# Kernel tuning notes

Hardware: AMD Instinct MI355X
Metric: run time of the kernel (lower is better)

The kernel has to match this reference:

```python
import jax, jax.numpy as jnp
import numpy as np
import math

SQRT2 = math.sqrt(2.0)


def _rotation_grids(theta_deg, grid_size):
    # torch affine_grid (align_corners=True) base coords for output [G, G]:
    # grid[h, w] = (xs[w], ys[h]) transformed by R = [[c, s, 0], [-s, c, 0]]
    xs = jnp.linspace(-1.0, 1.0, grid_size, dtype=jnp.float32)
    X, Y = jnp.meshgrid(xs, xs)            # [G,G], X varies along width
    th = jnp.deg2rad(theta_deg.astype(jnp.float32))[:, None, None]  # [T,1,1]
    c, s = jnp.cos(th), jnp.sin(th)
    gx = c * X + s * Y                      # [T,G,G]
    gy = -s * X + c * Y
    return gx, gy


def _bilinear_sample(x, gx, gy):
    # x: [N,C,H,W]; gx,gy: [T,G,G] normalized coords in [-1,1]
    # bilinear, zeros padding, align_corners=True -> returns [N,C,T,G,G]
    N, C, H, W = x.shape
    ix = (gx + 1.0) * 0.5 * (W - 1)
    iy = (gy + 1.0) * 0.5 * (H - 1)
    ix0 = jnp.floor(ix)
    iy0 = jnp.floor(iy)
    wx1 = ix - ix0
    wy1 = iy - iy0
    wx0 = 1.0 - wx1
    wy0 = 1.0 - wy1

    def gather(iyf, ixf):
        valid = (ixf >= 0) & (ixf <= W - 1) & (iyf >= 0) & (iyf <= H - 1)
        ii = jnp.clip(ixf, 0, W - 1).astype(jnp.int32)
        jj = jnp.clip(iyf, 0, H - 1).astype(jnp.int32)
        v = x[:, :, jj, ii]                 # [N,C,T,G,G]
        return v * valid.astype(x.dtype)

    return (gather(iy0, ix0) * (wy0 * wx0)
            + gather(iy0, ix0 + 1) * (wy0 * wx1)
            + gather(iy0 + 1, ix0) * (wy1 * wx0)
            + gather(iy0 + 1, ix0 + 1) * (wy1 * wx1))


def radon_forward(x, theta_deg):
    N, C, W, H = x.shape
    # circle=False: pad image to the diagonal size so rotations keep all content
    diagonal = SQRT2 * W
    pad = int(math.ceil(diagonal - W))
    new_center = (W + pad) // 2
    old_center = W // 2
    pad_before = new_center - old_center
    x = jnp.pad(x, ((0, 0), (0, 0), (pad_before, pad - pad_before),
                    (pad_before, pad - pad_before)))
    G = x.shape[-1]                         # padded grid size == ceil(sqrt2*W)
    gx, gy = _rotation_grids(theta_deg, G)  # [T,G,G]
    rotated = _bilinear_sample(x, gx, gy)   # [N,C,T,G,G]
    sino = rotated.sum(axis=3)              # integrate over rows -> [N,C,T,G]
    return jnp.swapaxes(sino, 2, 3)         # [N,C,G,T]


def setup_inputs() -> dict:
    key = jax.random.key(0)
    x = jax.random.normal(key, (2, 1, 256, 256), dtype=jnp.float32)
    theta = jnp.arange(180, dtype=jnp.int64) if jax.config.jax_enable_x64 else jnp.arange(180, dtype=jnp.int32)
    return {"x": x, "theta": theta}


def reference(x, theta):
    return radon_forward(x, theta)
```

## Files before the change

### kernel.cpp

```cpp
#include <hip/hip_runtime.h>
#include <hip/hip_fp16.h>
#include <math.h>


#define G       363
#define NT      180
#define PADB    53
#define STEP    (2.0f / 362.0f)
#define DEG2RAD 0.017453292519943295f

#define TS2     64
#define TROWS   68
#define NCHK    17
#define NTILE   (NCHK * 256)
#define NJB     12
#define NIB     8
#define NJBF    6
#define CW      264
#define CH      264
#define NTUPLE  (90 * NJB * NIB)

#define GLOAD16(gp, lp) __builtin_amdgcn_global_load_lds(                     \
    (const __attribute__((address_space(1))) void*)(gp),                      \
    (__attribute__((address_space(3))) void*)(lp), 16, 0, 0)

__global__ __launch_bounds__(256) void radon_fwd(
    const float* __restrict__ x, const int* __restrict__ theta,
    float* __restrict__ out)
{
    const int t = blockIdx.x / NJBF, jb = blockIdx.x % NJBF;
    const int jl = threadIdx.x, chunk = threadIdx.y;
    const int j = jb * 64 + jl;
    const float th = (float)theta[t] * DEG2RAD;
    const float c = cosf(th), s = sinf(th);
    const float xj = fmaf((float)j, STEP, -1.0f);
    const float s181 = s * 181.0f, c181 = c * 181.0f;
    const float bx = fmaf(c, xj, 1.0f) * 181.0f;
    const float by = fmaf(-s, xj, 1.0f) * 181.0f;
    const float* img0 = x;
    const float* img1 = x + 65536;
    float acc0 = 0.f, acc1 = 0.f;
    for (int i = chunk; i < G; i += 4) {
        const float xi = fmaf((float)i, STEP, -1.0f);
        const float ix = fmaf(s181, xi, bx);
        const float iy = fmaf(c181, xi, by);
        const float fx = floorf(ix), fy = floorf(iy);
        const int ix0 = (int)fx, iy0 = (int)fy;
        const float wx1 = ix - fx, wy1 = iy - fy;
        const float wx0 = 1.f - wx1, wy0 = 1.f - wy1;
        const int cc0 = ix0 - 53, cc1 = cc0 + 1, rr0 = iy0 - 53, rr1 = rr0 + 1;
        const float wxa = ((unsigned)cc0 < 256u) ? wx0 : 0.f;
        const float wxb = ((unsigned)cc1 < 256u) ? wx1 : 0.f;
        const float wya = ((unsigned)rr0 < 256u) ? wy0 : 0.f;
        const float wyb = ((unsigned)rr1 < 256u) ? wy1 : 0.f;
        const int c0c = min(max(cc0, 0), 255), c1c = min(max(cc1, 0), 255);
        const int r0b = min(max(rr0, 0), 255) << 8, r1b = min(max(rr1, 0), 255) << 8;
        const float w00 = wya * wxa, w01 = wya * wxb, w10 = wyb * wxa, w11 = wyb * wxb;
        acc0 = fmaf(img0[r0b + c0c], w00, acc0);
        acc0 = fmaf(img0[r0b + c1c], w01, acc0);
        acc0 = fmaf(img0[r1b + c0c], w10, acc0);
        acc0 = fmaf(img0[r1b + c1c], w11, acc0);
        acc1 = fmaf(img1[r0b + c0c], w00, acc1);
        acc1 = fmaf(img1[r0b + c1c], w01, acc1);
        acc1 = fmaf(img1[r1b + c0c], w10, acc1);
        acc1 = fmaf(img1[r1b + c1c], w11, acc1);
    }
    __shared__ float red[2][4][64];
    red[0][chunk][jl] = acc0;
    red[1][chunk][jl] = acc1;
    __syncthreads();
    if (threadIdx.y < 2 && j < G) {
        const int n = threadIdx.y;
        out[n * (G * NT) + j * NT + t] =
            red[n][0][jl] + red[n][1][jl] + red[n][2][jl] + red[n][3][jl];
    }
}

__global__ __launch_bounds__(256) void prep_k(
    const float* __restrict__ x, const int* __restrict__ theta,
    unsigned* __restrict__ xIh, unsigned* __restrict__ xTIh,
    int4* __restrict__ bbox, float* __restrict__ out)
{
    const int bid = blockIdx.x;
    const int tx = threadIdx.x, ty = threadIdx.y;
    const int tid = ty * 32 + tx;

    if (bid < 81) {
        __shared__ unsigned tl[32][33];
        const int cx0 = (bid % 9) * 32, cy0 = (bid / 9) * 32;
        #pragma unroll
        for (int dy = 0; dy < 32; dy += 8) {
            const int cy = cy0 + ty + dy, cx = cx0 + tx;
            const int pr = cy - 4, pc = cx - 4;
            unsigned v = 0u;
            if ((unsigned)pr < 256u && (unsigned)pc < 256u) {
                const int p = pr * 256 + pc;
                const unsigned short a = __half_as_ushort(__float2half_rn(x[p]));
                const unsigned short b = __half_as_ushort(__float2half_rn(x[p + 65536]));
                v = (unsigned)a | ((unsigned)b << 16);
            }
            if (cy < CH && cx < CW) xIh[cy * CW + cx] = v;
            tl[ty + dy][tx] = v;
        }
        __syncthreads();
        #pragma unroll
        for (int dy = 0; dy < 32; dy += 8) {
            const int rp = cx0 + ty + dy, cp = cy0 + tx;
            if (rp < CH && cp < CW) xTIh[rp * CW + cp] = tl[tx][ty + dy];
        }
    } else if (bid < 115) {
        const int tuple = (bid - 81) * 256 + tid;
        if (tuple < NTUPLE) {
            const int tg  = tuple / (NJB * NIB), rem = tuple - tg * (NJB * NIB);
            const int jb  = rem / NIB,   ib  = rem - jb * NIB;
            const float thA = (float)theta[tg * 2]     * DEG2RAD;
            const float thB = (float)theta[tg * 2 + 1] * DEG2RAD;
            const float cA = cosf(thA), sA = sinf(thA);
            const float cB = cosf(thB), sB = sinf(thB);
            const float xjm = fmaf((float)(jb * 32),      STEP, -1.0f);
            const float xjM = fmaf((float)(jb * 32 + 31), STEP, -1.0f);
            const float xim = fmaf((float)(ib * 48),      STEP, -1.0f);
            const float xiM = fmaf((float)(ib * 48 + 47), STEP, -1.0f);
            float ixmin = 1e30f, ixmax = -1e30f, iymin = 1e30f, iymax = -1e30f;
            #pragma unroll
            for (int qq = 0; qq < 8; ++qq) {
                const float cc  = (qq & 4) ? cB : cA;
                const float ss  = (qq & 4) ? sB : sA;
                const float xjc = (qq & 1) ? xjM : xjm;
                const float xic = (qq & 2) ? xiM : xim;
                const float bxq = fmaf(cc,  xjc, 1.0f) * 181.0f;
                const float byq = fmaf(-ss, xjc, 1.0f) * 181.0f;
                const float ixq = fmaf(ss * 181.0f, xic, bxq);
                const float iyq = fmaf(cc * 181.0f, xic, byq);
                ixmin = fminf(ixmin, ixq); ixmax = fmaxf(ixmax, ixq);
                iymin = fminf(iymin, iyq); iymax = fmaxf(iymax, iyq);
            }
            const int caseA = (fabsf(cA) + fabsf(cB) >= fabsf(sA) + fabsf(sB));
            const float Umin = caseA ? iymin : ixmin;
            const float Umax = caseA ? iymax : ixmax;
            const float Vmin = caseA ? ixmin : iymin;
            const int r0 = (int)floorf(Umin) - 1;
            const int c0 = (int)floorf(Vmin) - 1;
            int rows = (int)floorf(Umax) - (int)floorf(Umin) + 4;
            rows = min(rows, TROWS);
            const int nchunk = (rows + 3) >> 2;
            const int r0p = r0 - PADB, c0p = c0 - PADB;
            const int tyLast = (nchunk * 256 - 1) >> 6;
            const int safe = (r0p >= -4) && (r0p + tyLast <= 259)
                          && (c0p >= -4) && (c0p <= 196);
            bbox[tuple] = make_int4(r0p, c0p,
                                    nchunk | (safe << 8) | (caseA << 9),
                                    0);
        }
    } else {
        const int idx = (bid - 115) * 256 + tid;
        if (idx < 32670) ((float4*)out)[idx] = make_float4(0.f, 0.f, 0.f, 0.f);
    }
}

template<bool SAFE>
__device__ __forceinline__ void stage_direct(unsigned* tileB,
    const unsigned* __restrict__ srcC,
    int r0p, int c0p, int nchunk, int wid, int lane)
{
    const int B = (r0p + 4) * CW + (c0p + 4);
    for (int h = wid; h < nchunk; h += 4) {
        const int hs   = __builtin_amdgcn_readfirstlane(h);
        const int cell = (hs << 8) + (lane << 2);
        const int tyc  = cell >> 6;
        const int txc  = cell & 63;
        int idx;
        if (SAFE) {
            idx = tyc * CW + txc + B;
        } else {
            const int rc = min(max(r0p + tyc, -4), 256) + 4;
            const int cc = min(max(c0p + txc, -4), 256) + 4;
            idx = rc * CW + cc;
        }
        GLOAD16(srcC + idx, (char*)tileB + (hs << 10));
    }
}

template<bool TAIL>
__device__ __forceinline__ void gather6(const unsigned* __restrict__ tl,
    float Uf0, float Vf0, float dU, float dV, int iexc,
    float& a0, float& a1)
{
    __half2 acc = __float2half2_rn(0.0f);
    #pragma unroll
    for (int k = 0; k < 6; ++k) {
        const float Uf = fmaf((float)k, dU, Uf0);
        const float Vf = fmaf((float)k, dV, Vf0);
        const float fU = floorf(Uf), fV = floorf(Vf);
        const float wU1 = Uf - fU;
        const float wV1 = Vf - fV;
        const int rel = (int)fmaf(fU, (float)TS2, fV);
        const __half2 x00 = *(const __half2*)(tl + rel);
        const __half2 x01 = *(const __half2*)(tl + rel + 1);
        const __half2 x10 = *(const __half2*)(tl + rel + TS2);
        const __half2 x11 = *(const __half2*)(tl + rel + TS2 + 1);
        const __half2 wv2 = __float2half2_rn(wV1);
        const __half2 wu2 = __float2half2_rn(wU1);
        const __half2 t0 = __hfma2(wv2, __hsub2(x01, x00), x00);
        const __half2 t1 = __hfma2(wv2, __hsub2(x11, x10), x10);
        __half2 v = __hfma2(wu2, __hsub2(t1, t0), t0);
        if (TAIL && k >= iexc) v = __float2half2_rn(0.0f);
        acc = __hadd2(acc, v);
    }
    a0 += __low2float(acc);
    a1 += __high2float(acc);
}

__global__ __launch_bounds__(256) void radon_tile7(
    const unsigned* __restrict__ xIh, const unsigned* __restrict__ xTIh,
    const int*   __restrict__ theta, const int4* __restrict__ bbox,
    float* __restrict__ out)
{
    __shared__ unsigned tile[NTILE];

    const int blk  = blockIdx.x;
    const int z    = blockIdx.y;
    const int tg   = blk / NJB;
    const int jb   = blk - tg * NJB;
    const int tid  = threadIdx.x;
    const int lane = tid & 63;
    const int wid  = tid >> 6;
    const int a    = wid >> 1;
    const int wj   = wid & 1;
    const int jl   = lane & 15;
    const int kk   = lane >> 4;

    const int t = tg * 2 + a;
    const float th = (float)theta[t] * DEG2RAD;
    const float c = cosf(th), s = sinf(th);
    const float s181 = s * 181.0f, c181 = c * 181.0f;

    const int   j  = jb * 32 + wj * 16 + jl;
    const float xj = fmaf((float)j, STEP, -1.0f);
    const float bx = fmaf(c,  xj, 1.0f) * 181.0f;
    const float by = fmaf(-s, xj, 1.0f) * 181.0f;

    const float fiofs = (float)(kk * 12);

    const int tb = (tg * NJB + jb) * NIB + z * 4;
    const int caseA = (__builtin_amdgcn_readfirstlane(bbox[tb].z) >> 9) & 1;
    const unsigned* __restrict__ srcC = caseA ? xIh : xTIh;

    const float slopeU = caseA ? c181 : s181;
    const float slopeV = caseA ? s181 : c181;
    const float dU = slopeU * STEP;
    const float dV = slopeV * STEP;
    const float U00 = (caseA ? by : bx) - slopeU;
    const float V00 = (caseA ? bx : by) - slopeV;

    float a0 = 0.f, a1 = 0.f;

    #pragma unroll
    for (int ibi = 0; ibi < 4; ++ibi) {
        const int ib = z * 4 + ibi;
        const int4 bb = bbox[tb + ibi];
        const int r0p    = __builtin_amdgcn_readfirstlane(bb.x);
        const int c0p    = __builtin_amdgcn_readfirstlane(bb.y);
        const int flags  = __builtin_amdgcn_readfirstlane(bb.z);
        const int nchunk = flags & 255;
        const int safe   = (flags >> 8) & 1;

        __syncthreads();

        if (safe) stage_direct<true >(tile, srcC, r0p, c0p, nchunk, wid, lane);
        else      stage_direct<false>(tile, srcC, r0p, c0p, nchunk, wid, lane);
        __syncthreads();

        const int i0 = ib * 48;
        const float r0f = (float)(r0p + PADB);
        const float c0f = (float)(c0p + PADB);
        const float fi  = (float)i0 + fiofs;
        const float Uf1 = fmaf(dU, fi, U00) - r0f;
        const float Vf1 = fmaf(dV, fi, V00) - c0f;
        const float Uf2 = fmaf(dU, 6.0f, Uf1);
        const float Vf2 = fmaf(dV, 6.0f, Vf1);
        const int ibase = i0 + kk * 12;

        if (i0 + 47 < G) {
            gather6<false>(tile, Uf1, Vf1, dU, dV, 6, a0, a1);
            gather6<false>(tile, Uf2, Vf2, dU, dV, 6, a0, a1);
        } else {
            gather6<true>(tile, Uf1, Vf1, dU, dV, G - ibase,     a0, a1);
            gather6<true>(tile, Uf2, Vf2, dU, dV, G - ibase - 6, a0, a1);
        }
    }

    float vx = a0;
    float vy = a1;
    vx += __shfl_xor(vx, 16);
    vy += __shfl_xor(vy, 16);
    vx += __shfl_xor(vx, 32);
    vy += __shfl_xor(vy, 32);

    if (lane < 16 && j < G) {
        atomicAdd(&out[j * NT + t],          vx);
        atomicAdd(&out[G * NT + j * NT + t], vy);
    }
}

extern "C" void kernel_launch(void* const* d_in, const int* in_sizes, int n_in,
                              void* d_out, int out_size, void* d_ws, size_t ws_size,
                              hipStream_t stream) {
    const float* x     = (const float*)d_in[0];
    const int*   theta = (const int*)d_in[1];
    float*       out   = (float*)d_out;

    const size_t XIH_OFF  = 0;
    const size_t XTIH_OFF = (size_t)CH * CW * 4;
    const size_t BBOX_OFF = 2 * XTIH_OFF;
    const size_t NEED     = BBOX_OFF + (size_t)NTUPLE * 16;

    if (ws_size < NEED) {
        hipLaunchKernelGGL(radon_fwd, dim3(NT * NJBF), dim3(64, 4), 0, stream,
                           x, theta, out);
        return;
    }

    unsigned* xIh  = (unsigned*)((char*)d_ws + XIH_OFF);
    unsigned* xTIh = (unsigned*)((char*)d_ws + XTIH_OFF);
    int4*     bbox = (int4*)((char*)d_ws + BBOX_OFF);

    hipLaunchKernelGGL(prep_k, dim3(243), dim3(32, 8), 0, stream,
                       x, theta, xIh, xTIh, bbox, out);
    hipLaunchKernelGGL(radon_tile7, dim3(1080, 2), dim3(256), 0, stream,
                       xIh, xTIh, theta, bbox, out);
}
```

Baseline: 34.06 us.

## Replace LDS-tiled bbox staging with direct L2 gathers from padded half images

```diff
diff --git a/kernel.cpp b/kernel.cpp
--- a/kernel.cpp
+++ b/kernel.cpp
@@ -5,24 +5,13 @@
 
 #define G       363
 #define NT      180
-#define PADB    53
 #define STEP    (2.0f / 362.0f)
 #define DEG2RAD 0.017453292519943295f
 
-#define TS2     64
-#define TROWS   68
-#define NCHK    17
-#define NTILE   (NCHK * 256)
 #define NJB     12
-#define NIB     8
 #define NJBF    6
 #define CW      264
 #define CH      264
-#define NTUPLE  (90 * NJB * NIB)
-
-#define GLOAD16(gp, lp) __builtin_amdgcn_global_load_lds(                     \
-    (const __attribute__((address_space(1))) void*)(gp),                      \
-    (__attribute__((address_space(3))) void*)(lp), 16, 0, 0)
 
 __global__ __launch_bounds__(256) void radon_fwd(
     const float* __restrict__ x, const int* __restrict__ theta,
@@ -77,229 +66,133 @@
 }
 
 __global__ __launch_bounds__(256) void prep_k(
-    const float* __restrict__ x, const int* __restrict__ theta,
-    unsigned* __restrict__ xIh, unsigned* __restrict__ xTIh,
-    int4* __restrict__ bbox, float* __restrict__ out)
+    const float* __restrict__ x,
+    unsigned* __restrict__ xIh, unsigned* __restrict__ xTIh)
 {
     const int bid = blockIdx.x;
     const int tx = threadIdx.x, ty = threadIdx.y;
-    const int tid = ty * 32 + tx;
-
-    if (bid < 81) {
-        __shared__ unsigned tl[32][33];
-        const int cx0 = (bid % 9) * 32, cy0 = (bid / 9) * 32;
-        #pragma unroll
-        for (int dy = 0; dy < 32; dy += 8) {
-            const int cy = cy0 + ty + dy, cx = cx0 + tx;
-            const int pr = cy - 4, pc = cx - 4;
-            unsigned v = 0u;
-            if ((unsigned)pr < 256u && (unsigned)pc < 256u) {
-                const int p = pr * 256 + pc;
-                const unsigned short a = __half_as_ushort(__float2half_rn(x[p]));
-                const unsigned short b = __half_as_ushort(__float2half_rn(x[p + 65536]));
-                v = (unsigned)a | ((unsigned)b << 16);
-            }
-            if (cy < CH && cx < CW) xIh[cy * CW + cx] = v;
-            tl[ty + dy][tx] = v;
+
+    __shared__ unsigned tl[32][33];
+    const int cx0 = (bid % 9) * 32, cy0 = (bid / 9) * 32;
+    #pragma unroll
+    for (int dy = 0; dy < 32; dy += 8) {
+        const int cy = cy0 + ty + dy, cx = cx0 + tx;
+        const int pr = cy - 4, pc = cx - 4;
+        unsigned v = 0u;
+        if ((unsigned)pr < 256u && (unsigned)pc < 256u) {
+            const int p = pr * 256 + pc;
+            const unsigned short a = __half_as_ushort(__float2half_rn(x[p]));
+            const unsigned short b = __half_as_ushort(__float2half_rn(x[p + 65536]));
+            v = (unsigned)a | ((unsigned)b << 16);
         }
-        __syncthreads();
-        #pragma unroll
-        for (int dy = 0; dy < 32; dy += 8) {
-            const int rp = cx0 + ty + dy, cp = cy0 + tx;
-            if (rp < CH && cp < CW) xTIh[rp * CW + cp] = tl[tx][ty + dy];
-        }
-    } else if (bid < 115) {
-        const int tuple = (bid - 81) * 256 + tid;
-        if (tuple < NTUPLE) {
-            const int tg  = tuple / (NJB * NIB), rem = tuple - tg * (NJB * NIB);
-            const int jb  = rem / NIB,   ib  = rem - jb * NIB;
-            const float thA = (float)theta[tg * 2]     * DEG2RAD;
-            const float thB = (float)theta[tg * 2 + 1] * DEG2RAD;
-            const float cA = cosf(thA), sA = sinf(thA);
-            const float cB = cosf(thB), sB = sinf(thB);
-            const float xjm = fmaf((float)(jb * 32),      STEP, -1.0f);
-            const float xjM = fmaf((float)(jb * 32 + 31), STEP, -1.0f);
-            const float xim = fmaf((float)(ib * 48),      STEP, -1.0f);
-            const float xiM = fmaf((float)(ib * 48 + 47), STEP, -1.0f);
-            float ixmin = 1e30f, ixmax = -1e30f, iymin = 1e30f, iymax = -1e30f;
-            #pragma unroll
-            for (int qq = 0; qq < 8; ++qq) {
-                const float cc  = (qq & 4) ? cB : cA;
-                const float ss  = (qq & 4) ? sB : sA;
-                const float xjc = (qq & 1) ? xjM : xjm;
-                const float xic = (qq & 2) ? xiM : xim;
-                const float bxq = fmaf(cc,  xjc, 1.0f) * 181.0f;
-                const float byq = fmaf(-ss, xjc, 1.0f) * 181.0f;
-                const float ixq = fmaf(ss * 181.0f, xic, bxq);
-                const float iyq = fmaf(cc * 181.0f, xic, byq);
-                ixmin = fminf(ixmin, ixq); ixmax = fmaxf(ixmax, ixq);
-                iymin = fminf(iymin, iyq); iymax = fmaxf(iymax, iyq);
-            }
-            const int caseA = (fabsf(cA) + fabsf(cB) >= fabsf(sA) + fabsf(sB));
-            const float Umin = caseA ? iymin : ixmin;
-            const float Umax = caseA ? iymax : ixmax;
-            const float Vmin = caseA ? ixmin : iymin;
-            const int r0 = (int)floorf(Umin) - 1;
-            const int c0 = (int)floorf(Vmin) - 1;
-            int rows = (int)floorf(Umax) - (int)floorf(Umin) + 4;
-            rows = min(rows, TROWS);
-            const int nchunk = (rows + 3) >> 2;
-            const int r0p = r0 - PADB, c0p = c0 - PADB;
-            const int tyLast = (nchunk * 256 - 1) >> 6;
-            const int safe = (r0p >= -4) && (r0p + tyLast <= 259)
-                          && (c0p >= -4) && (c0p <= 196);
-            bbox[tuple] = make_int4(r0p, c0p,
-                                    nchunk | (safe << 8) | (caseA << 9),
-                                    0);
-        }
-    } else {
-        const int idx = (bid - 115) * 256 + tid;
-        if (idx < 32670) ((float4*)out)[idx] = make_float4(0.f, 0.f, 0.f, 0.f);
-    }
-}
-
-template<bool SAFE>
-__device__ __forceinline__ void stage_direct(unsigned* tileB,
-    const unsigned* __restrict__ srcC,
-    int r0p, int c0p, int nchunk, int wid, int lane)
-{
-    const int B = (r0p + 4) * CW + (c0p + 4);
-    for (int h = wid; h < nchunk; h += 4) {
-        const int hs   = __builtin_amdgcn_readfirstlane(h);
-        const int cell = (hs << 8) + (lane << 2);
-        const int tyc  = cell >> 6;
-        const int txc  = cell & 63;
-        int idx;
-        if (SAFE) {
-            idx = tyc * CW + txc + B;
-        } else {
-            const int rc = min(max(r0p + tyc, -4), 256) + 4;
-            const int cc = min(max(c0p + txc, -4), 256) + 4;
-            idx = rc * CW + cc;
-        }
-        GLOAD16(srcC + idx, (char*)tileB + (hs << 10));
-    }
-}
-
-template<bool TAIL>
-__device__ __forceinline__ void gather6(const unsigned* __restrict__ tl,
-    float Uf0, float Vf0, float dU, float dV, int iexc,
-    float& a0, float& a1)
-{
-    __half2 acc = __float2half2_rn(0.0f);
+        if (cy < CH && cx < CW) xIh[cy * CW + cx] = v;
+        tl[ty + dy][tx] = v;
+    }
+    __syncthreads();
     #pragma unroll
-    for (int k = 0; k < 6; ++k) {
-        const float Uf = fmaf((float)k, dU, Uf0);
-        const float Vf = fmaf((float)k, dV, Vf0);
-        const float fU = floorf(Uf), fV = floorf(Vf);
-        const float wU1 = Uf - fU;
-        const float wV1 = Vf - fV;
-        const int rel = (int)fmaf(fU, (float)TS2, fV);
-        const __half2 x00 = *(const __half2*)(tl + rel);
-        const __half2 x01 = *(const __half2*)(tl + rel + 1);
-        const __half2 x10 = *(const __half2*)(tl + rel + TS2);
-        const __half2 x11 = *(const __half2*)(tl + rel + TS2 + 1);
-        const __half2 wv2 = __float2half2_rn(wV1);
-        const __half2 wu2 = __float2half2_rn(wU1);
-        const __half2 t0 = __hfma2(wv2, __hsub2(x01, x00), x00);
-        const __half2 t1 = __hfma2(wv2, __hsub2(x11, x10), x10);
-        __half2 v = __hfma2(wu2, __hsub2(t1, t0), t0);
-        if (TAIL && k >= iexc) v = __float2half2_rn(0.0f);
-        acc = __hadd2(acc, v);
-    }
-    a0 += __low2float(acc);
-    a1 += __high2float(acc);
-}
-
-__global__ __launch_bounds__(256) void radon_tile7(
+    for (int dy = 0; dy < 32; dy += 8) {
+        const int rp = cx0 + ty + dy, cp = cy0 + tx;
+        if (rp < CH && cp < CW) xTIh[rp * CW + cp] = tl[tx][ty + dy];
+    }
+}
+
+__device__ __forceinline__ __half2 tap(const unsigned* __restrict__ cv,
+    float fi, float dU, float dV, float U00, float V00)
+{
+    const float U = fmaf(dU, fi, U00);
+    const float V = fmaf(dV, fi, V00);
+    const float fU = floorf(U), fV = floorf(V);
+    const float wU1 = U - fU, wV1 = V - fV;
+    const float fUc = fminf(fmaxf(fU, 0.0f), 262.0f);
+    const float fVc = fminf(fmaxf(fV, 0.0f), 262.0f);
+    const int rel = (int)fmaf(fUc, (float)CW, fVc);
+    const __half2* p = (const __half2*)(cv + rel);
+    const __half2 x00 = p[0];
+    const __half2 x01 = p[1];
+    const __half2 x10 = p[CW];
+    const __half2 x11 = p[CW + 1];
+    const __half2 wv2 = __float2half2_rn(wV1);
+    const __half2 wu2 = __float2half2_rn(wU1);
+    const __half2 t0 = __hfma2(wv2, __hsub2(x01, x00), x00);
+    const __half2 t1 = __hfma2(wv2, __hsub2(x11, x10), x10);
+    return __hfma2(wu2, __hsub2(t1, t0), t0);
+}
+
+__global__ __launch_bounds__(256) void radon_l2(
     const unsigned* __restrict__ xIh, const unsigned* __restrict__ xTIh,
-    const int*   __restrict__ theta, const int4* __restrict__ bbox,
-    float* __restrict__ out)
-{
-    __shared__ unsigned tile[NTILE];
-
+    const int* __restrict__ theta, float* __restrict__ out)
+{
     const int blk  = blockIdx.x;
-    const int z    = blockIdx.y;
-    const int tg   = blk / NJB;
-    const int jb   = blk - tg * NJB;
+    const int t    = blk / NJB;
+    const int jb   = blk - t * NJB;
     const int tid  = threadIdx.x;
     const int lane = tid & 63;
     const int wid  = tid >> 6;
-    const int a    = wid >> 1;
-    const int wj   = wid & 1;
-    const int jl   = lane & 15;
-    const int kk   = lane >> 4;
-
-    const int t = tg * 2 + a;
+    const int jl   = lane & 31;
+    const int kc   = lane >> 5;
+    const int chunk = wid * 2 + kc;
+
     const float th = (float)theta[t] * DEG2RAD;
     const float c = cosf(th), s = sinf(th);
     const float s181 = s * 181.0f, c181 = c * 181.0f;
 
-    const int   j  = jb * 32 + wj * 16 + jl;
+    const int   j  = jb * 32 + jl;
     const float xj = fmaf((float)j, STEP, -1.0f);
     const float bx = fmaf(c,  xj, 1.0f) * 181.0f;
     const float by = fmaf(-s, xj, 1.0f) * 181.0f;
 
-    const float fiofs = (float)(kk * 12);
-
-    const int tb = (tg * NJB + jb) * NIB + z * 4;
-    const int caseA = (__builtin_amdgcn_readfirstlane(bbox[tb].z) >> 9) & 1;
-    const unsigned* __restrict__ srcC = caseA ? xIh : xTIh;
+    const int caseA = (fabsf(c) >= fabsf(s));
+    const unsigned* __restrict__ cv = caseA ? xIh : xTIh;
 
     const float slopeU = caseA ? c181 : s181;
     const float slopeV = caseA ? s181 : c181;
     const float dU = slopeU * STEP;
     const float dV = slopeV * STEP;
-    const float U00 = (caseA ? by : bx) - slopeU;
-    const float V00 = (caseA ? bx : by) - slopeV;
+    const float U00 = (caseA ? by : bx) - slopeU - 49.0f;
+    const float V00 = (caseA ? bx : by) - slopeV - 49.0f;
 
     float a0 = 0.f, a1 = 0.f;
 
-    #pragma unroll
-    for (int ibi = 0; ibi < 4; ++ibi) {
-        const int ib = z * 4 + ibi;
-        const int4 bb = bbox[tb + ibi];
-        const int r0p    = __builtin_amdgcn_readfirstlane(bb.x);
-        const int c0p    = __builtin_amdgcn_readfirstlane(bb.y);
-        const int flags  = __builtin_amdgcn_readfirstlane(bb.z);
-        const int nchunk = flags & 255;
-        const int safe   = (flags >> 8) & 1;
-
-        __syncthreads();
-
-        if (safe) stage_direct<true >(tile, srcC, r0p, c0p, nchunk, wid, lane);
-        else      stage_direct<false>(tile, srcC, r0p, c0p, nchunk, wid, lane);
-        __syncthreads();
-
-        const int i0 = ib * 48;
-        const float r0f = (float)(r0p + PADB);
-        const float c0f = (float)(c0p + PADB);
-        const float fi  = (float)i0 + fiofs;
-        const float Uf1 = fmaf(dU, fi, U00) - r0f;
-        const float Vf1 = fmaf(dV, fi, V00) - c0f;
-        const float Uf2 = fmaf(dU, 6.0f, Uf1);
-        const float Vf2 = fmaf(dV, 6.0f, Vf1);
-        const int ibase = i0 + kk * 12;
-
-        if (i0 + 47 < G) {
-            gather6<false>(tile, Uf1, Vf1, dU, dV, 6, a0, a1);
-            gather6<false>(tile, Uf2, Vf2, dU, dV, 6, a0, a1);
-        } else {
-            gather6<true>(tile, Uf1, Vf1, dU, dV, G - ibase,     a0, a1);
-            gather6<true>(tile, Uf2, Vf2, dU, dV, G - ibase - 6, a0, a1);
+    float fig = (float)chunk;
+    for (int g = 0; g < 7; ++g) {
+        __half2 acc = __float2half2_rn(0.0f);
+        #pragma unroll
+        for (int k = 0; k < 6; ++k) {
+            acc = __hadd2(acc, tap(cv, fig + (float)(k * 8), dU, dV, U00, V00));
         }
-    }
-
-    float vx = a0;
-    float vy = a1;
-    vx += __shfl_xor(vx, 16);
-    vy += __shfl_xor(vy, 16);
-    vx += __shfl_xor(vx, 32);
-    vy += __shfl_xor(vy, 32);
-
-    if (lane < 16 && j < G) {
-        atomicAdd(&out[j * NT + t],          vx);
-        atomicAdd(&out[G * NT + j * NT + t], vy);
+        a0 += __low2float(acc);
+        a1 += __high2float(acc);
+        fig += 48.0f;
+    }
+    {
+        __half2 acc = __float2half2_rn(0.0f);
+        #pragma unroll
+        for (int k = 42; k < 46; ++k) {
+            const int i = chunk + k * 8;
+            if (i < G)
+                acc = __hadd2(acc, tap(cv, (float)i, dU, dV, U00, V00));
+        }
+        a0 += __low2float(acc);
+        a1 += __high2float(acc);
+    }
+
+    a0 += __shfl_xor(a0, 32);
+    a1 += __shfl_xor(a1, 32);
+
+    __shared__ float red[2][4][32];
+    if (lane < 32) {
+        red[0][wid][jl] = a0;
+        red[1][wid][jl] = a1;
+    }
+    __syncthreads();
+
+    if (tid < 64) {
+        const int n = tid >> 5, jj = tid & 31;
+        const float v = red[n][0][jj] + red[n][1][jj]
+                      + red[n][2][jj] + red[n][3][jj];
+        const int jo = jb * 32 + jj;
+        if (jo < G)
+            out[(n * G + jo) * NT + t] = v;
     }
 }
 
@@ -312,8 +205,7 @@
 
     const size_t XIH_OFF  = 0;
     const size_t XTIH_OFF = (size_t)CH * CW * 4;
-    const size_t BBOX_OFF = 2 * XTIH_OFF;
-    const size_t NEED     = BBOX_OFF + (size_t)NTUPLE * 16;
+    const size_t NEED     = 2 * XTIH_OFF;
 
     if (ws_size < NEED) {
         hipLaunchKernelGGL(radon_fwd, dim3(NT * NJBF), dim3(64, 4), 0, stream,
@@ -323,10 +215,9 @@
 
     unsigned* xIh  = (unsigned*)((char*)d_ws + XIH_OFF);
     unsigned* xTIh = (unsigned*)((char*)d_ws + XTIH_OFF);
-    int4*     bbox = (int4*)((char*)d_ws + BBOX_OFF);
-
-    hipLaunchKernelGGL(prep_k, dim3(243), dim3(32, 8), 0, stream,
-                       x, theta, xIh, xTIh, bbox, out);
-    hipLaunchKernelGGL(radon_tile7, dim3(1080, 2), dim3(256), 0, stream,
-                       xIh, xTIh, theta, bbox, out);
-}
+
+    hipLaunchKernelGGL(prep_k, dim3(81), dim3(32, 8), 0, stream,
+                       x, xIh, xTIh);
+    hipLaunchKernelGGL(radon_l2, dim3(NT * NJB), dim3(256), 0, stream,
+                       xIh, xTIh, theta, out);
+}
```

After: 39.10 us. 1.15x slower.
